# Kernel optimization log

Hardware: AMD Instinct MI355X
Metric: run time of the kernel (lower is better)

Reference implementation:

```python
import jax, jax.numpy as jnp
import numpy as np

NUM_FIELDS = 40
# upper-triangular (i<j) field pair indices, computed once at trace time
_I_IDX, _J_IDX = np.triu_indices(NUM_FIELDS, k=1)  # each length 780


def setup_inputs() -> dict:
    key = jax.random.key(0)
    k1, k2 = jax.random.split(key)
    batch, num_fields, embed_dim = 8192, NUM_FIELDS, 32
    num_interactions = num_fields * (num_fields - 1) // 2  # 780
    embeddings = jax.random.normal(k1, (batch, num_fields, embed_dim), dtype=jnp.float32)
    W = jax.random.normal(k2, (num_interactions, embed_dim, embed_dim), dtype=jnp.float32)
    return {"embeddings": embeddings, "W": W}


def reference(embeddings, W):
    # embeddings: (b, f, e); W: (k, e, e) with k = f*(f-1)/2
    vi = embeddings[:, _I_IDX, :]  # (b, k, e)
    vj = embeddings[:, _J_IDX, :]  # (b, k, e)
    # per-pair bilinear form, reduced over embed dims -> (b, k)
    return jnp.einsum('bke,kef,bkf->bk', vi, W, vj)
```

## Files before the change

kernel.cpp:

```cpp
#include <hip/hip_runtime.h>
#include <cstdint>
#include <cstddef>

typedef __attribute__((ext_vector_type(8))) short short8;
typedef __attribute__((ext_vector_type(4))) unsigned short ushort4_t;
typedef __attribute__((ext_vector_type(16))) float f32x16;

#define NF 40
#define NK 780
#define BT 32
#define THREADS 1024

__device__ __forceinline__ unsigned short f2bf(float f) {
    unsigned int u = __float_as_uint(f);
    u = (u + 0x7fffu + ((u >> 16) & 1u)) >> 16;
    return (unsigned short)u;
}
__device__ __forceinline__ float bf2f(unsigned short x) {
    return __uint_as_float(((unsigned int)x) << 16);
}

__global__ __launch_bounds__(128) void wprep_kernel(const float* __restrict__ W,
                                                    unsigned short* __restrict__ wfrag) {
    const int k = blockIdx.x, t = threadIdx.x;
    const int half = t >> 6, l = t & 63;
    const int e = l & 31;
    const int f0 = 16 * half + 8 * (l >> 5);
    const float* src = W + (size_t)k * 1024 + e * 32 + f0;
    const float4 x0 = *(const float4*)src;
    const float4 x1 = *(const float4*)(src + 4);
    short8 v;
    v[0] = (short)f2bf(x0.x); v[1] = (short)f2bf(x0.y);
    v[2] = (short)f2bf(x0.z); v[3] = (short)f2bf(x0.w);
    v[4] = (short)f2bf(x1.x); v[5] = (short)f2bf(x1.y);
    v[6] = (short)f2bf(x1.z); v[7] = (short)f2bf(x1.w);
    *(short8*)(wfrag + (size_t)k * 1024 + half * 512 + l * 8) = v;
}

__device__ __forceinline__ void ld_w4(short8& r0, short8& r1, short8& r2, short8& r3,
                                      const char* addr) {
    asm volatile("global_load_dwordx4 %0, %4, off\n\t"
                 "global_load_dwordx4 %1, %4, off offset:1024\n\t"
                 "global_load_dwordx4 %2, %4, off offset:2048\n\t"
                 "global_load_dwordx4 %3, %4, off offset:3072"
                 : "=&v"(r0), "=&v"(r1), "=&v"(r2), "=&v"(r3)
                 : "v"(addr));
}
#define WAITP() do { asm volatile("s_waitcnt vmcnt(4)" ::: "memory"); \
                     __builtin_amdgcn_sched_barrier(0); } while (0)
#define WAIT0() do { asm volatile("s_waitcnt vmcnt(0)" ::: "memory"); \
                     __builtin_amdgcn_sched_barrier(0); } while (0)

#define LOADW2(R0, R1, R2, R3, KB)                                                      \
    {                                                                                   \
        const int kbc = (KB) > 778 ? 778 : (KB);                                        \
        ld_w4(R0, R1, R2, R3, wbase + ((size_t)kbc << 11));                             \
    }


#define RELOAD_VI()                                                                     \
    {                                                                                   \
        const int i7 = ii & 7;                                                          \
        const char* ibase = embT + (ii << 11) + eoff;                                   \
        const ushort4_t r0 = *(const ushort4_t*)(ibase + (((b32     ) ^ i7) << 4));     \
        const ushort4_t r1 = *(const ushort4_t*)(ibase + (((b32 + 32) ^ i7) << 4));     \
        const ushort4_t r2 = *(const ushort4_t*)(ibase + (((b32 + 64) ^ i7) << 4));     \
        const ushort4_t r3 = *(const ushort4_t*)(ibase + (((b32 + 96) ^ i7) << 4));     \
        vf0  = bf2f(r0[0]); vf1  = bf2f(r0[1]); vf2  = bf2f(r0[2]); vf3  = bf2f(r0[3]); \
        vf4  = bf2f(r1[0]); vf5  = bf2f(r1[1]); vf6  = bf2f(r1[2]); vf7  = bf2f(r1[3]); \
        vf8  = bf2f(r2[0]); vf9  = bf2f(r2[1]); vf10 = bf2f(r2[2]); vf11 = bf2f(r2[3]); \
        vf12 = bf2f(r3[0]); vf13 = bf2f(r3[1]); vf14 = bf2f(r3[2]); vf15 = bf2f(r3[3]); \
    }

#define KSTEP(A0, A1, OREG)                                                             \
    {                                                                                   \
        const int j7 = jj & 7;                                                          \
        const char* jbase = embT + (jj << 11);                                          \
        const short8 vj0 = *(const short8*)(jbase + (((b32 + fq0) ^ j7) << 4));         \
        const short8 vj1 = *(const short8*)(jbase + (((b32 + fq1) ^ j7) << 4));         \
        f32x16 t = {};                                                                  \
        t = __builtin_amdgcn_mfma_f32_32x32x16_bf16(A0, vj0, t, 0, 0, 0);               \
        t = __builtin_amdgcn_mfma_f32_32x32x16_bf16(A1, vj1, t, 0, 0, 0);               \
        float p = t[0]*vf0  + t[1]*vf1  + t[2]*vf2   + t[3]*vf3                         \
                + t[4]*vf4  + t[5]*vf5  + t[6]*vf6   + t[7]*vf7                         \
                + t[8]*vf8  + t[9]*vf9  + t[10]*vf10 + t[11]*vf11                       \
                + t[12]*vf12+ t[13]*vf13+ t[14]*vf14 + t[15]*vf15;                      \
        p += __shfl_xor(p, 32);                                                         \
        OREG = p;                                                                       \
        ++jj;                                                                           \
        if (jj == NF) { ++ii; jj = ii + 1; RELOAD_VI(); }                               \
    }

#define STEP2(KNEXT, C0, C1, C2, C3, N0, N1, N2, N3, OA, OB)                            \
    LOADW2(N0, N1, N2, N3, KNEXT);                                                      \
    WAITP();                                                                            \
    KSTEP(C0, C1, OA);                                                                  \
    KSTEP(C2, C3, OB);

__global__ __launch_bounds__(THREADS) void bil_kernel(const float* __restrict__ emb,
                                                      const unsigned short* __restrict__ wfrag,
                                                      float* __restrict__ out) {
    __shared__ __align__(16) char embT[NF * 2048];

    const int tid = threadIdx.x;
    const int b0 = blockIdx.x * BT;

    for (int u = tid; u < BT * 160; u += THREADS) {
        const int bb = u / 160;
        const int t = u - 160 * bb;
        const int field = t >> 2;
        const int fq = t & 3;
        const float* src = emb + (size_t)(b0 + bb) * (NF * 32) + field * 32 + 8 * fq;
        const float4 x0 = *(const float4*)src;
        const float4 x1 = *(const float4*)(src + 4);
        short8 v;
        v[0] = (short)f2bf(x0.x); v[1] = (short)f2bf(x0.y);
        v[2] = (short)f2bf(x0.z); v[3] = (short)f2bf(x0.w);
        v[4] = (short)f2bf(x1.x); v[5] = (short)f2bf(x1.y);
        v[6] = (short)f2bf(x1.z); v[7] = (short)f2bf(x1.w);
        const int g = (bb + 32 * fq) ^ (field & 7);
        *(short8*)(embT + field * 2048 + g * 16) = v;
    }
    __syncthreads();

    const int ww = tid >> 6;
    const int l = tid & 63;
    const int b32 = l & 31;
    const int h32 = l >> 5;
    const int fq0 = 32 * h32;
    const int fq1 = 64 + 32 * h32;
    const int eoff = 8 * h32;

    const int ks = 4 * ((195 * ww) >> 4);
    const int ke = 4 * ((195 * (ww + 1)) >> 4);

    int ii = 0, jj;
    {
        int kk = ks, len = 39;
        while (kk >= len) { kk -= len; ++ii; --len; }
        jj = ii + 1 + kk;
    }

    float vf0, vf1, vf2, vf3, vf4, vf5, vf6, vf7;
    float vf8, vf9, vf10, vf11, vf12, vf13, vf14, vf15;
    RELOAD_VI();

    const char* wbase = (const char*)wfrag + l * 16;

    short8 a0, a1, a2, a3;
    short8 bb0, bb1, bb2, bb3;
    LOADW2(a0, a1, a2, a3, ks);

    int kcur = ks;
    while (kcur + 16 <= ke) {
        float o0, o1, o2, o3, o4, o5, o6, o7;
        float o8, o9, o10, o11, o12, o13, o14, o15;
        STEP2(kcur + 2,  a0, a1, a2, a3, bb0, bb1, bb2, bb3, o0,  o1)
        STEP2(kcur + 4,  bb0, bb1, bb2, bb3, a0, a1, a2, a3, o2,  o3)
        STEP2(kcur + 6,  a0, a1, a2, a3, bb0, bb1, bb2, bb3, o4,  o5)
        STEP2(kcur + 8,  bb0, bb1, bb2, bb3, a0, a1, a2, a3, o6,  o7)
        STEP2(kcur + 10, a0, a1, a2, a3, bb0, bb1, bb2, bb3, o8,  o9)
        STEP2(kcur + 12, bb0, bb1, bb2, bb3, a0, a1, a2, a3, o10, o11)
        STEP2(kcur + 14, a0, a1, a2, a3, bb0, bb1, bb2, bb3, o12, o13)
        STEP2(kcur + 16, bb0, bb1, bb2, bb3, a0, a1, a2, a3, o14, o15)
        if (l < 32) {
            float* orow = out + (size_t)(b0 + l) * NK + kcur;
            float4 s;
            s.x = o0;  s.y = o1;  s.z = o2;  s.w = o3;  *(float4*)(orow)      = s;
            s.x = o4;  s.y = o5;  s.z = o6;  s.w = o7;  *(float4*)(orow + 4)  = s;
            s.x = o8;  s.y = o9;  s.z = o10; s.w = o11; *(float4*)(orow + 8)  = s;
            s.x = o12; s.y = o13; s.z = o14; s.w = o15; *(float4*)(orow + 12) = s;
        }
        kcur += 16;
    }
    if (kcur < ke) {
        float o0, o1, o2, o3;
        LOADW2(bb0, bb1, bb2, bb3, kcur + 2);
        WAITP();
        KSTEP(a0, a1, o0);
        KSTEP(a2, a3, o1);
        WAIT0();
        KSTEP(bb0, bb1, o2);
        KSTEP(bb2, bb3, o3);
        if (l < 32) {
            float4 s; s.x = o0; s.y = o1; s.z = o2; s.w = o3;
            *(float4*)(out + (size_t)(b0 + l) * NK + kcur) = s;
        }
    }
}

extern "C" void kernel_launch(void* const* d_in, const int* in_sizes, int n_in,
                              void* d_out, int out_size, void* d_ws, size_t ws_size,
                              hipStream_t stream) {
    const float* emb = (const float*)d_in[0];
    const float* W   = (const float*)d_in[1];
    float* out = (float*)d_out;
    unsigned short* wfrag = (unsigned short*)d_ws;

    wprep_kernel<<<dim3(NK), dim3(128), 0, stream>>>(W, wfrag);
    bil_kernel<<<dim3(8192 / BT), dim3(THREADS), 0, stream>>>(emb, wfrag, out);
}
```

Baseline: 41.75 us.

## Process 64 batch rows per block, reusing each W fragment for two MFMA tiles

Doubles the batch tile per block from 32 to 64 rows, so every W fragment loaded from global memory feeds two 32x32 MFMA tiles (A and B halves). This halves total W traffic and the number of blocks. The shared embedding buffer doubles to 160KB with an adjusted swizzle, and both half-waves now write output rows instead of only half. The 16-wide unrolled loop is replaced by a 4-step loop, and the dot reduction is split into four FMA chains. The costs are more registers, larger LDS, fewer blocks (128) on the device, and unclear occupancy.

```diff
diff --git a/kernel.cpp b/kernel.cpp
--- a/kernel.cpp
+++ b/kernel.cpp
@@ -8,7 +8,7 @@
 
 #define NF 40
 #define NK 780
-#define BT 32
+#define BT 64
 #define THREADS 1024
 
 __device__ __forceinline__ unsigned short f2bf(float f) {
@@ -48,8 +48,6 @@
 }
 #define WAITP() do { asm volatile("s_waitcnt vmcnt(4)" ::: "memory"); \
                      __builtin_amdgcn_sched_barrier(0); } while (0)
-#define WAIT0() do { asm volatile("s_waitcnt vmcnt(0)" ::: "memory"); \
-                     __builtin_amdgcn_sched_barrier(0); } while (0)
 
 #define LOADW2(R0, R1, R2, R3, KB)                                                      \
     {                                                                                   \
@@ -61,46 +59,71 @@
 #define RELOAD_VI()                                                                     \
     {                                                                                   \
         const int i7 = ii & 7;                                                          \
-        const char* ibase = embT + (ii << 11) + eoff;                                   \
-        const ushort4_t r0 = *(const ushort4_t*)(ibase + (((b32     ) ^ i7) << 4));     \
-        const ushort4_t r1 = *(const ushort4_t*)(ibase + (((b32 + 32) ^ i7) << 4));     \
-        const ushort4_t r2 = *(const ushort4_t*)(ibase + (((b32 + 64) ^ i7) << 4));     \
-        const ushort4_t r3 = *(const ushort4_t*)(ibase + (((b32 + 96) ^ i7) << 4));     \
-        vf0  = bf2f(r0[0]); vf1  = bf2f(r0[1]); vf2  = bf2f(r0[2]); vf3  = bf2f(r0[3]); \
-        vf4  = bf2f(r1[0]); vf5  = bf2f(r1[1]); vf6  = bf2f(r1[2]); vf7  = bf2f(r1[3]); \
-        vf8  = bf2f(r2[0]); vf9  = bf2f(r2[1]); vf10 = bf2f(r2[2]); vf11 = bf2f(r2[3]); \
-        vf12 = bf2f(r3[0]); vf13 = bf2f(r3[1]); vf14 = bf2f(r3[2]); vf15 = bf2f(r3[3]); \
-    }
-
-#define KSTEP(A0, A1, OREG)                                                             \
+        const char* ibase = embT + (ii << 12) + eoff;                                   \
+        const ushort4_t a0_ = *(const ushort4_t*)(ibase + (((b32      ) ^ i7) << 4));   \
+        const ushort4_t a1_ = *(const ushort4_t*)(ibase + (((b32 +  64) ^ i7) << 4));   \
+        const ushort4_t a2_ = *(const ushort4_t*)(ibase + (((b32 + 128) ^ i7) << 4));   \
+        const ushort4_t a3_ = *(const ushort4_t*)(ibase + (((b32 + 192) ^ i7) << 4));   \
+        const ushort4_t b0_ = *(const ushort4_t*)(ibase + (((b32 +  32) ^ i7) << 4));   \
+        const ushort4_t b1_ = *(const ushort4_t*)(ibase + (((b32 +  96) ^ i7) << 4));   \
+        const ushort4_t b2_ = *(const ushort4_t*)(ibase + (((b32 + 160) ^ i7) << 4));   \
+        const ushort4_t b3_ = *(const ushort4_t*)(ibase + (((b32 + 224) ^ i7) << 4));   \
+        uA0 = bf2f(a0_[0]); uA1 = bf2f(a0_[1]); uA2  = bf2f(a0_[2]); uA3  = bf2f(a0_[3]); \
+        uA4 = bf2f(a1_[0]); uA5 = bf2f(a1_[1]); uA6  = bf2f(a1_[2]); uA7  = bf2f(a1_[3]); \
+        uA8 = bf2f(a2_[0]); uA9 = bf2f(a2_[1]); uA10 = bf2f(a2_[2]); uA11 = bf2f(a2_[3]); \
+        uA12 = bf2f(a3_[0]); uA13 = bf2f(a3_[1]); uA14 = bf2f(a3_[2]); uA15 = bf2f(a3_[3]); \
+        uB0 = bf2f(b0_[0]); uB1 = bf2f(b0_[1]); uB2  = bf2f(b0_[2]); uB3  = bf2f(b0_[3]); \
+        uB4 = bf2f(b1_[0]); uB5 = bf2f(b1_[1]); uB6  = bf2f(b1_[2]); uB7  = bf2f(b1_[3]); \
+        uB8 = bf2f(b2_[0]); uB9 = bf2f(b2_[1]); uB10 = bf2f(b2_[2]); uB11 = bf2f(b2_[3]); \
+        uB12 = bf2f(b3_[0]); uB13 = bf2f(b3_[1]); uB14 = bf2f(b3_[2]); uB15 = bf2f(b3_[3]); \
+    }
+
+#define DOT16(T, V0, V1, V2, V3, V4, V5, V6, V7, V8, V9, V10, V11, V12, V13, V14, V15, P) \
+    {                                                                                   \
+        float c0 = T[0] * V0;                                                           \
+        c0 = __builtin_fmaf(T[1], V1, c0);                                              \
+        c0 = __builtin_fmaf(T[2], V2, c0);                                              \
+        c0 = __builtin_fmaf(T[3], V3, c0);                                              \
+        float c1 = T[4] * V4;                                                           \
+        c1 = __builtin_fmaf(T[5], V5, c1);                                              \
+        c1 = __builtin_fmaf(T[6], V6, c1);                                              \
+        c1 = __builtin_fmaf(T[7], V7, c1);                                              \
+        float c2 = T[8] * V8;                                                           \
+        c2 = __builtin_fmaf(T[9], V9, c2);                                              \
+        c2 = __builtin_fmaf(T[10], V10, c2);                                            \
+        c2 = __builtin_fmaf(T[11], V11, c2);                                            \
+        float c3 = T[12] * V12;                                                         \
+        c3 = __builtin_fmaf(T[13], V13, c3);                                            \
+        c3 = __builtin_fmaf(T[14], V14, c3);                                            \
+        c3 = __builtin_fmaf(T[15], V15, c3);                                            \
+        P = (c0 + c1) + (c2 + c3);                                                      \
+        P += __shfl_xor(P, 32);                                                         \
+    }
+
+#define KSTEP(A0, A1, OA, OB)                                                           \
     {                                                                                   \
         const int j7 = jj & 7;                                                          \
-        const char* jbase = embT + (jj << 11);                                          \
-        const short8 vj0 = *(const short8*)(jbase + (((b32 + fq0) ^ j7) << 4));         \
-        const short8 vj1 = *(const short8*)(jbase + (((b32 + fq1) ^ j7) << 4));         \
-        f32x16 t = {};                                                                  \
-        t = __builtin_amdgcn_mfma_f32_32x32x16_bf16(A0, vj0, t, 0, 0, 0);               \
-        t = __builtin_amdgcn_mfma_f32_32x32x16_bf16(A1, vj1, t, 0, 0, 0);               \
-        float p = t[0]*vf0  + t[1]*vf1  + t[2]*vf2   + t[3]*vf3                         \
-                + t[4]*vf4  + t[5]*vf5  + t[6]*vf6   + t[7]*vf7                         \
-                + t[8]*vf8  + t[9]*vf9  + t[10]*vf10 + t[11]*vf11                       \
-                + t[12]*vf12+ t[13]*vf13+ t[14]*vf14 + t[15]*vf15;                      \
-        p += __shfl_xor(p, 32);                                                         \
-        OREG = p;                                                                       \
+        const char* jbase = embT + (jj << 12);                                          \
+        const short8 vjA0 = *(const short8*)(jbase + (((b32 +       fh0) ^ j7) << 4));  \
+        const short8 vjA1 = *(const short8*)(jbase + (((b32 + 128 + fh0) ^ j7) << 4));  \
+        const short8 vjB0 = *(const short8*)(jbase + (((b32 + 32  + fh0) ^ j7) << 4));  \
+        const short8 vjB1 = *(const short8*)(jbase + (((b32 + 160 + fh0) ^ j7) << 4));  \
+        f32x16 tA = __builtin_amdgcn_mfma_f32_32x32x16_bf16(A0, vjA0, zacc, 0, 0, 0);   \
+        tA = __builtin_amdgcn_mfma_f32_32x32x16_bf16(A1, vjA1, tA, 0, 0, 0);            \
+        f32x16 tB = __builtin_amdgcn_mfma_f32_32x32x16_bf16(A0, vjB0, zacc, 0, 0, 0);   \
+        tB = __builtin_amdgcn_mfma_f32_32x32x16_bf16(A1, vjB1, tB, 0, 0, 0);            \
+        DOT16(tA, uA0, uA1, uA2, uA3, uA4, uA5, uA6, uA7,                               \
+                  uA8, uA9, uA10, uA11, uA12, uA13, uA14, uA15, OA);                    \
+        DOT16(tB, uB0, uB1, uB2, uB3, uB4, uB5, uB6, uB7,                               \
+                  uB8, uB9, uB10, uB11, uB12, uB13, uB14, uB15, OB);                    \
         ++jj;                                                                           \
         if (jj == NF) { ++ii; jj = ii + 1; RELOAD_VI(); }                               \
     }
 
-#define STEP2(KNEXT, C0, C1, C2, C3, N0, N1, N2, N3, OA, OB)                            \
-    LOADW2(N0, N1, N2, N3, KNEXT);                                                      \
-    WAITP();                                                                            \
-    KSTEP(C0, C1, OA);                                                                  \
-    KSTEP(C2, C3, OB);
-
-__global__ __launch_bounds__(THREADS) void bil_kernel(const float* __restrict__ emb,
-                                                      const unsigned short* __restrict__ wfrag,
-                                                      float* __restrict__ out) {
-    __shared__ __align__(16) char embT[NF * 2048];
+__global__ __launch_bounds__(THREADS, 4) void bil_kernel(const float* __restrict__ emb,
+                                                         const unsigned short* __restrict__ wfrag,
+                                                         float* __restrict__ out) {
+    __shared__ __align__(16) char embT[NF * 4096];
 
     const int tid = threadIdx.x;
     const int b0 = blockIdx.x * BT;
@@ -118,8 +141,8 @@
         v[2] = (short)f2bf(x0.z); v[3] = (short)f2bf(x0.w);
         v[4] = (short)f2bf(x1.x); v[5] = (short)f2bf(x1.y);
         v[6] = (short)f2bf(x1.z); v[7] = (short)f2bf(x1.w);
-        const int g = (bb + 32 * fq) ^ (field & 7);
-        *(short8*)(embT + field * 2048 + g * 16) = v;
+        const int g = (bb + 64 * fq) ^ (field & 7);
+        *(short8*)(embT + field * 4096 + g * 16) = v;
     }
     __syncthreads();
 
@@ -127,9 +150,10 @@
     const int l = tid & 63;
     const int b32 = l & 31;
     const int h32 = l >> 5;
-    const int fq0 = 32 * h32;
-    const int fq1 = 64 + 32 * h32;
+    const int fh0 = 64 * h32;
     const int eoff = 8 * h32;
+
+    const f32x16 zacc = {};
 
     const int ks = 4 * ((195 * ww) >> 4);
     const int ke = 4 * ((195 * (ww + 1)) >> 4);
@@ -141,51 +165,34 @@
         jj = ii + 1 + kk;
     }
 
-    float vf0, vf1, vf2, vf3, vf4, vf5, vf6, vf7;
-    float vf8, vf9, vf10, vf11, vf12, vf13, vf14, vf15;
+    float uA0, uA1, uA2, uA3, uA4, uA5, uA6, uA7;
+    float uA8, uA9, uA10, uA11, uA12, uA13, uA14, uA15;
+    float uB0, uB1, uB2, uB3, uB4, uB5, uB6, uB7;
+    float uB8, uB9, uB10, uB11, uB12, uB13, uB14, uB15;
     RELOAD_VI();
 
     const char* wbase = (const char*)wfrag + l * 16;
 
     short8 a0, a1, a2, a3;
-    short8 bb0, bb1, bb2, bb3;
+    short8 c0, c1, c2, c3;
     LOADW2(a0, a1, a2, a3, ks);
 
-    int kcur = ks;
-    while (kcur + 16 <= ke) {
-        float o0, o1, o2, o3, o4, o5, o6, o7;
-        float o8, o9, o10, o11, o12, o13, o14, o15;
-        STEP2(kcur + 2,  a0, a1, a2, a3, bb0, bb1, bb2, bb3, o0,  o1)
-        STEP2(kcur + 4,  bb0, bb1, bb2, bb3, a0, a1, a2, a3, o2,  o3)
-        STEP2(kcur + 6,  a0, a1, a2, a3, bb0, bb1, bb2, bb3, o4,  o5)
-        STEP2(kcur + 8,  bb0, bb1, bb2, bb3, a0, a1, a2, a3, o6,  o7)
-        STEP2(kcur + 10, a0, a1, a2, a3, bb0, bb1, bb2, bb3, o8,  o9)
-        STEP2(kcur + 12, bb0, bb1, bb2, bb3, a0, a1, a2, a3, o10, o11)
-        STEP2(kcur + 14, a0, a1, a2, a3, bb0, bb1, bb2, bb3, o12, o13)
-        STEP2(kcur + 16, bb0, bb1, bb2, bb3, a0, a1, a2, a3, o14, o15)
-        if (l < 32) {
-            float* orow = out + (size_t)(b0 + l) * NK + kcur;
-            float4 s;
-            s.x = o0;  s.y = o1;  s.z = o2;  s.w = o3;  *(float4*)(orow)      = s;
-            s.x = o4;  s.y = o5;  s.z = o6;  s.w = o7;  *(float4*)(orow + 4)  = s;
-            s.x = o8;  s.y = o9;  s.z = o10; s.w = o11; *(float4*)(orow + 8)  = s;
-            s.x = o12; s.y = o13; s.z = o14; s.w = o15; *(float4*)(orow + 12) = s;
-        }
-        kcur += 16;
-    }
-    if (kcur < ke) {
-        float o0, o1, o2, o3;
-        LOADW2(bb0, bb1, bb2, bb3, kcur + 2);
+    const size_t orowoff = (size_t)(b0 + 32 * h32 + b32) * NK;
+
+    for (int kcur = ks; kcur < ke; kcur += 4) {
+        float oA0, oA1, oA2, oA3, oB0, oB1, oB2, oB3;
+        LOADW2(c0, c1, c2, c3, kcur + 2);
         WAITP();
-        KSTEP(a0, a1, o0);
-        KSTEP(a2, a3, o1);
-        WAIT0();
-        KSTEP(bb0, bb1, o2);
-        KSTEP(bb2, bb3, o3);
-        if (l < 32) {
-            float4 s; s.x = o0; s.y = o1; s.z = o2; s.w = o3;
-            *(float4*)(out + (size_t)(b0 + l) * NK + kcur) = s;
-        }
+        KSTEP(a0, a1, oA0, oB0);
+        KSTEP(a2, a3, oA1, oB1);
+        LOADW2(a0, a1, a2, a3, kcur + 4);
+        WAITP();
+        KSTEP(c0, c1, oA2, oB2);
+        KSTEP(c2, c3, oA3, oB3);
+        float4 s;
+        if (h32 == 0) { s.x = oA0; s.y = oA1; s.z = oA2; s.w = oA3; }
+        else          { s.x = oB0; s.y = oB1; s.z = oB2; s.w = oB3; }
+        *(float4*)(out + orowoff + kcur) = s;
     }
 }
 
```

Result: slower. 48.17 us (+15.4%).
